# Performance work log

Measured on AMD Instinct MI355X. Metric: run time of the kernel, lower is better.

The kernel has to match this reference:

```python
import jax, jax.numpy as jnp
import numpy as np

B = 500_000
N = 6          # n_neurons
STEPS = 10     # spiking update loop length
SUBSTEPS = 8   # TwoCompColumn substeps
NOISE_STD = 0.3
I_TONIC = -1.0
# Izhikevich 'RS' parameters
IZ_A, IZ_B, IZ_C, IZ_D = 0.02, 0.2, -65.0, 8.0
V_THRESH = 30.0
RATE_ALPHA = 0.1   # rate EMA
PC_TAU = 0.5       # compartment relaxation rate


def setup_inputs() -> dict:
    key = jax.random.key(0)
    k = jax.random.split(key, 8)
    heading = jax.random.normal(k[0], (B,), dtype=jnp.float32)
    speed = jax.random.uniform(k[1], (B,), dtype=jnp.float32)
    turn_rate = jax.random.normal(k[2], (B,), dtype=jnp.float32)
    predicted_turn = jax.random.normal(k[3], (B,), dtype=jnp.float32)
    predicted_speed = jax.random.uniform(k[4], (B,), dtype=jnp.float32)
    noise = jax.random.normal(k[5], (STEPS, B, N), dtype=jnp.float32)
    # Izhikevich resting state around v=-65, u=b*v, with small jitter
    v0 = -65.0 + 2.0 * jax.random.normal(k[6], (B, N), dtype=jnp.float32)
    u0 = IZ_B * v0
    rate0 = jnp.zeros((B, N), dtype=jnp.float32)
    return {
        "heading": heading, "speed": speed, "turn_rate": turn_rate,
        "predicted_turn": predicted_turn, "predicted_speed": predicted_speed,
        "noise": noise, "v0": v0, "u0": u0, "rate0": rate0,
    }


def reference(heading, speed, turn_rate, predicted_turn, predicted_speed,
              noise, v0, u0, rate0):
    # heading is carried for API fidelity; original forward never uses it.
    del heading
    tilt = jnp.minimum(1.0, jnp.abs(turn_rate) * speed * 0.5)          # [B]
    zero = jnp.float32(0.0)
    I = jnp.stack([
        jnp.maximum(zero, turn_rate) * 10.0,
        jnp.maximum(zero, -turn_rate) * 10.0,
        speed * 5.0,
        jnp.maximum(zero, -speed + 0.5) * 5.0,
        tilt * 8.0,
        tilt * 8.0,
    ], axis=-1)                                                        # [B, N]

    def izh_step(carry, nz):
        v, u, r = carry                                                # each [B, N]
        i_tot = I + nz * NOISE_STD + I_TONIC
        v = v + (0.04 * v * v + 5.0 * v + 140.0 - u + i_tot)
        u = u + IZ_A * (IZ_B * v - u)
        fired = v >= V_THRESH
        spk = fired.astype(v.dtype)
        v = jnp.where(fired, IZ_C, v)
        u = u + spk * IZ_D
        r = r * (1.0 - RATE_ALPHA) + spk * RATE_ALPHA
        return (v, u, r), None

    (_, _, rate), _ = jax.lax.scan(izh_step, (v0, u0, rate0), noise)
    rate_mean = jnp.mean(rate, axis=-1)                                # [B]

    # TwoCompColumn: basal tracks sensory, apical tracks prediction
    sensory = jnp.stack([turn_rate, speed], axis=-1)                   # [B, 2]
    prediction = jnp.stack([predicted_turn, predicted_speed], axis=-1) # [B, 2]

    def pc_step(carry, _):
        vb, va = carry
        vb = vb + PC_TAU * (sensory - vb)
        va = va + PC_TAU * (prediction - va)
        return (vb, va), None

    (vb, va), _ = jax.lax.scan(pc_step,
                               (jnp.zeros_like(sensory), jnp.zeros_like(prediction)),
                               None, length=SUBSTEPS)
    pe = vb - va                                                       # [B, 2]
    precision = 1.0 / (1.0 + pe * pe)                                  # [B, 2]
    free_energy = 0.5 * jnp.sum(precision * pe * pe, axis=-1)          # [B]
    pe_w = 0.7 * pe[..., 0] + 0.3 * pe[..., 1]                         # [B]
    prec_mean = jnp.mean(precision, axis=-1)                           # [B]
    postural = -prec_mean * pe_w * 0.3                                 # [B]

    # [B, 6]: (tilt, rate, postural_correction, prediction_error, precision, free_energy)
    return jnp.stack([tilt, rate_mean, postural, pe_w, prec_mean, free_energy], axis=-1)
```

## Files before the change

### kernel.cpp

```cpp
#include <hip/hip_runtime.h>

#define STEPS 10
#define NN 6

__global__ __launch_bounds__(256) void spiking_vestibular_kernel(
    const float* __restrict__ speed,
    const float* __restrict__ turn_rate,
    const float* __restrict__ predicted_turn,
    const float* __restrict__ predicted_speed,
    const float* __restrict__ noise,
    const float* __restrict__ v0,
    const float* __restrict__ u0,
    const float* __restrict__ rate0,
    float* __restrict__ out,
    int B)
{
#pragma clang fp contract(off)
    int b = blockIdx.x * blockDim.x + threadIdx.x;
    if (b >= B) return;

    float tr = turn_rate[b];
    float sp = speed[b];
    float pt = predicted_turn[b];
    float ps = predicted_speed[b];

    float tilt = fminf(1.0f, fabsf(tr) * sp * 0.5f);

    float I[NN];
    I[0] = fmaxf(0.0f, tr) * 10.0f;
    I[1] = fmaxf(0.0f, -tr) * 10.0f;
    I[2] = sp * 5.0f;
    I[3] = fmaxf(0.0f, -sp + 0.5f) * 5.0f;
    I[4] = tilt * 8.0f;
    I[5] = tilt * 8.0f;

    size_t base6 = (size_t)b * NN;

    float v[NN], u[NN], r[NN];
    {
        const float2* p = reinterpret_cast<const float2*>(v0 + base6);
        float2 a0 = p[0], a1 = p[1], a2 = p[2];
        v[0] = a0.x; v[1] = a0.y; v[2] = a1.x; v[3] = a1.y; v[4] = a2.x; v[5] = a2.y;
    }
    {
        const float2* p = reinterpret_cast<const float2*>(u0 + base6);
        float2 a0 = p[0], a1 = p[1], a2 = p[2];
        u[0] = a0.x; u[1] = a0.y; u[2] = a1.x; u[3] = a1.y; u[4] = a2.x; u[5] = a2.y;
    }
    {
        const float2* p = reinterpret_cast<const float2*>(rate0 + base6);
        float2 a0 = p[0], a1 = p[1], a2 = p[2];
        r[0] = a0.x; r[1] = a0.y; r[2] = a1.x; r[3] = a1.y; r[4] = a2.x; r[5] = a2.y;
    }

    for (int t = 0; t < STEPS; ++t) {
        const float2* p = reinterpret_cast<const float2*>(noise + ((size_t)t * (size_t)B + (size_t)b) * NN);
        float2 n0 = p[0], n1 = p[1], n2 = p[2];
        float nz[NN] = { n0.x, n0.y, n1.x, n1.y, n2.x, n2.y };
#pragma unroll
        for (int n = 0; n < NN; ++n) {
            float i_tot = I[n] + nz[n] * 0.3f + (-1.0f);
            float vv = v[n];
            float un = u[n];
            vv = vv + (((((0.04f * vv) * vv) + (5.0f * vv)) + 140.0f) - un + i_tot);
            un = un + 0.02f * ((0.2f * vv) - un);
            bool fired = (vv >= 30.0f);
            float spk = fired ? 1.0f : 0.0f;
            vv = fired ? -65.0f : vv;
            un = un + spk * 8.0f;
            r[n] = r[n] * 0.9f + spk * 0.1f;
            v[n] = vv;
            u[n] = un;
        }
    }

    float rsum = ((((r[0] + r[1]) + r[2]) + r[3]) + r[4]) + r[5];
    float rate_mean = rsum / 6.0f;

    float vb0 = 0.0f, vb1 = 0.0f, va0 = 0.0f, va1 = 0.0f;
#pragma unroll
    for (int k = 0; k < 8; ++k) {
        vb0 = vb0 + 0.5f * (tr - vb0);
        vb1 = vb1 + 0.5f * (sp - vb1);
        va0 = va0 + 0.5f * (pt - va0);
        va1 = va1 + 0.5f * (ps - va1);
    }
    float pe0 = vb0 - va0;
    float pe1 = vb1 - va1;
    float prec0 = 1.0f / (1.0f + pe0 * pe0);
    float prec1 = 1.0f / (1.0f + pe1 * pe1);
    float fe = 0.5f * (((prec0 * pe0) * pe0) + ((prec1 * pe1) * pe1));
    float pe_w = 0.7f * pe0 + 0.3f * pe1;
    float prec_mean = (prec0 + prec1) / 2.0f;
    float postural = (-prec_mean) * pe_w * 0.3f;

    float2* o = reinterpret_cast<float2*>(out + base6);
    o[0] = make_float2(tilt, rate_mean);
    o[1] = make_float2(postural, pe_w);
    o[2] = make_float2(prec_mean, fe);
}

extern "C" void kernel_launch(void* const* d_in, const int* in_sizes, int n_in,
                              void* d_out, int out_size, void* d_ws, size_t ws_size,
                              hipStream_t stream) {
    const float* speed           = (const float*)d_in[1];
    const float* turn_rate       = (const float*)d_in[2];
    const float* predicted_turn  = (const float*)d_in[3];
    const float* predicted_speed = (const float*)d_in[4];
    const float* noise           = (const float*)d_in[5];
    const float* v0              = (const float*)d_in[6];
    const float* u0              = (const float*)d_in[7];
    const float* rate0           = (const float*)d_in[8];
    float* out                   = (float*)d_out;

    int B = in_sizes[1];
    int block = 256;
    int grid = (B + block - 1) / block;
    spiking_vestibular_kernel<<<grid, block, 0, stream>>>(
        speed, turn_rate, predicted_turn, predicted_speed,
        noise, v0, u0, rate0, out, B);
}
```

Baseline: 221.9 us.

## Split each batch element across four lanes handling neuron pairs

Each batch element is now processed by four threads. Three of them each own a pair of neurons, and the fourth duplicates the first pair's work, so the wave stays aligned. All noise loads are hoisted ahead of the loop so they can be in flight together, and the rate sum is reduced with lane shuffles. This gives more parallelism and lanes reading contiguous float2 data, which should coalesce memory traffic better in this memory-bound kernel. The cost is one quarter of the lanes doing wasted work, plus a redundant prediction-error computation in every lane.

Measured after the change: 219.2 us. Within noise of the previous version (-1.2%).

```diff
diff --git a/kernel.cpp b/kernel.cpp
--- a/kernel.cpp
+++ b/kernel.cpp
@@ -1,7 +1,6 @@
 #include <hip/hip_runtime.h>
 
 #define STEPS 10
-#define NN 6
 
 __global__ __launch_bounds__(256) void spiking_vestibular_kernel(
     const float* __restrict__ speed,
@@ -16,77 +15,85 @@
     int B)
 {
 #pragma clang fp contract(off)
-    int b = blockIdx.x * blockDim.x + threadIdx.x;
+    int tid = blockIdx.x * blockDim.x + threadIdx.x;
+    int b = tid >> 2;
+    int g = tid & 3;
     if (b >= B) return;
+
+    size_t base6 = (size_t)b * 6;
+    int goff = (g == 3) ? 0 : (2 * g);
+
+    float2 nz[STEPS];
+#pragma unroll
+    for (int t = 0; t < STEPS; ++t)
+        nz[t] = *reinterpret_cast<const float2*>(noise + (size_t)t * (size_t)B * 6 + base6 + goff);
+
+    float2 v2 = *reinterpret_cast<const float2*>(v0    + base6 + goff);
+    float2 u2 = *reinterpret_cast<const float2*>(u0    + base6 + goff);
+    float2 r2 = *reinterpret_cast<const float2*>(rate0 + base6 + goff);
 
     float tr = turn_rate[b];
     float sp = speed[b];
     float pt = predicted_turn[b];
     float ps = predicted_speed[b];
 
-    float tilt = fminf(1.0f, fabsf(tr) * sp * 0.5f);
+    float tilt = fminf(1.0f, (fabsf(tr) * sp) * 0.5f);
 
-    float I[NN];
-    I[0] = fmaxf(0.0f, tr) * 10.0f;
-    I[1] = fmaxf(0.0f, -tr) * 10.0f;
-    I[2] = sp * 5.0f;
-    I[3] = fmaxf(0.0f, -sp + 0.5f) * 5.0f;
-    I[4] = tilt * 8.0f;
-    I[5] = tilt * 8.0f;
+    float t8 = tilt * 8.0f;
+    float Ia = (g == 0) ? fmaxf(0.0f, tr) * 10.0f
+             : (g == 1) ? sp * 5.0f
+             : t8;
+    float Ib = (g == 0) ? fmaxf(0.0f, -tr) * 10.0f
+             : (g == 1) ? fmaxf(0.0f, -sp + 0.5f) * 5.0f
+             : t8;
 
-    size_t base6 = (size_t)b * NN;
+    float va = v2.x, vb = v2.y;
+    float ua = u2.x, ub = u2.y;
+    float ra = r2.x, rb = r2.y;
 
-    float v[NN], u[NN], r[NN];
-    {
-        const float2* p = reinterpret_cast<const float2*>(v0 + base6);
-        float2 a0 = p[0], a1 = p[1], a2 = p[2];
-        v[0] = a0.x; v[1] = a0.y; v[2] = a1.x; v[3] = a1.y; v[4] = a2.x; v[5] = a2.y;
-    }
-    {
-        const float2* p = reinterpret_cast<const float2*>(u0 + base6);
-        float2 a0 = p[0], a1 = p[1], a2 = p[2];
-        u[0] = a0.x; u[1] = a0.y; u[2] = a1.x; u[3] = a1.y; u[4] = a2.x; u[5] = a2.y;
-    }
-    {
-        const float2* p = reinterpret_cast<const float2*>(rate0 + base6);
-        float2 a0 = p[0], a1 = p[1], a2 = p[2];
-        r[0] = a0.x; r[1] = a0.y; r[2] = a1.x; r[3] = a1.y; r[4] = a2.x; r[5] = a2.y;
-    }
-
+#pragma unroll
     for (int t = 0; t < STEPS; ++t) {
-        const float2* p = reinterpret_cast<const float2*>(noise + ((size_t)t * (size_t)B + (size_t)b) * NN);
-        float2 n0 = p[0], n1 = p[1], n2 = p[2];
-        float nz[NN] = { n0.x, n0.y, n1.x, n1.y, n2.x, n2.y };
-#pragma unroll
-        for (int n = 0; n < NN; ++n) {
-            float i_tot = I[n] + nz[n] * 0.3f + (-1.0f);
-            float vv = v[n];
-            float un = u[n];
+        {
+            float i_tot = Ia + nz[t].x * 0.3f + (-1.0f);
+            float vv = va, un = ua;
             vv = vv + (((((0.04f * vv) * vv) + (5.0f * vv)) + 140.0f) - un + i_tot);
             un = un + 0.02f * ((0.2f * vv) - un);
             bool fired = (vv >= 30.0f);
             float spk = fired ? 1.0f : 0.0f;
             vv = fired ? -65.0f : vv;
             un = un + spk * 8.0f;
-            r[n] = r[n] * 0.9f + spk * 0.1f;
-            v[n] = vv;
-            u[n] = un;
+            ra = ra * 0.9f + spk * 0.1f;
+            va = vv; ua = un;
+        }
+        {
+            float i_tot = Ib + nz[t].y * 0.3f + (-1.0f);
+            float vv = vb, un = ub;
+            vv = vv + (((((0.04f * vv) * vv) + (5.0f * vv)) + 140.0f) - un + i_tot);
+            un = un + 0.02f * ((0.2f * vv) - un);
+            bool fired = (vv >= 30.0f);
+            float spk = fired ? 1.0f : 0.0f;
+            vv = fired ? -65.0f : vv;
+            un = un + spk * 8.0f;
+            rb = rb * 0.9f + spk * 0.1f;
+            vb = vv; ub = un;
         }
     }
 
-    float rsum = ((((r[0] + r[1]) + r[2]) + r[3]) + r[4]) + r[5];
-    float rate_mean = rsum / 6.0f;
+    float s  = ra + rb;
+    float s1 = __shfl_down(s, 1, 4);
+    float s2 = __shfl_down(s, 2, 4);
+    float rate_mean = ((s + s1) + s2) / 6.0f;
 
-    float vb0 = 0.0f, vb1 = 0.0f, va0 = 0.0f, va1 = 0.0f;
+    float cb0 = 0.0f, cb1 = 0.0f, ca0 = 0.0f, ca1 = 0.0f;
 #pragma unroll
     for (int k = 0; k < 8; ++k) {
-        vb0 = vb0 + 0.5f * (tr - vb0);
-        vb1 = vb1 + 0.5f * (sp - vb1);
-        va0 = va0 + 0.5f * (pt - va0);
-        va1 = va1 + 0.5f * (ps - va1);
+        cb0 = cb0 + 0.5f * (tr - cb0);
+        cb1 = cb1 + 0.5f * (sp - cb1);
+        ca0 = ca0 + 0.5f * (pt - ca0);
+        ca1 = ca1 + 0.5f * (ps - ca1);
     }
-    float pe0 = vb0 - va0;
-    float pe1 = vb1 - va1;
+    float pe0 = cb0 - ca0;
+    float pe1 = cb1 - ca1;
     float prec0 = 1.0f / (1.0f + pe0 * pe0);
     float prec1 = 1.0f / (1.0f + pe1 * pe1);
     float fe = 0.5f * (((prec0 * pe0) * pe0) + ((prec1 * pe1) * pe1));
@@ -94,10 +101,12 @@
     float prec_mean = (prec0 + prec1) / 2.0f;
     float postural = (-prec_mean) * pe_w * 0.3f;
 
-    float2* o = reinterpret_cast<float2*>(out + base6);
-    o[0] = make_float2(tilt, rate_mean);
-    o[1] = make_float2(postural, pe_w);
-    o[2] = make_float2(prec_mean, fe);
+    if (g < 3) {
+        float2 o = (g == 0) ? make_float2(tilt, rate_mean)
+                 : (g == 1) ? make_float2(postural, pe_w)
+                 :            make_float2(prec_mean, fe);
+        *reinterpret_cast<float2*>(out + base6 + 2 * g) = o;
+    }
 }
 
 extern "C" void kernel_launch(void* const* d_in, const int* in_sizes, int n_in,
@@ -114,8 +123,9 @@
     float* out                   = (float*)d_out;
 
     int B = in_sizes[1];
+    long long total = (long long)B * 4;
     int block = 256;
-    int grid = (B + block - 1) / block;
+    int grid = (int)((total + block - 1) / block);
     spiking_vestibular_kernel<<<grid, block, 0, stream>>>(
         speed, turn_rate, predicted_turn, predicted_speed,
         noise, v0, u0, rate0, out, B);
```

## Stage noise and state through LDS with async global_load_lds double buffering

Applied to the files above, without the earlier changes.

Replaces per-thread strided float2 loads of noise, v0, u0 and rate0 with wave-cooperative 16-byte global_load_lds copies into shared-memory slabs. Noise timesteps are double-buffered, with the load for step t+2 issued after step t finishes. The goal is fully coalesced global reads and overlap of memory traffic with compute. In exchange it adds a block-wide barrier every step, uses 60KB of LDS per 512-thread block (which limits occupancy), and clamps tail chunk addresses.

Result: slower. 227.6 us (+2.6%).

```diff
diff --git a/kernel.cpp b/kernel.cpp
--- a/kernel.cpp
+++ b/kernel.cpp
@@ -1,9 +1,18 @@
 #include <hip/hip_runtime.h>
 
 #define STEPS 10
-#define NN 6
+#define EPB 512
+#define BLOCK 512
+#define SLAB_F 3072
+#define CHUNK_F 256
+#define NCHUNK 12
 
-__global__ __launch_bounds__(256) void spiking_vestibular_kernel(
+#define GLOAD_LDS16(gp, lp)                                            \
+    __builtin_amdgcn_global_load_lds(                                  \
+        (const __attribute__((address_space(1))) void*)(gp),           \
+        (__attribute__((address_space(3))) void*)(lp), 16, 0, 0)
+
+__global__ __launch_bounds__(BLOCK) void spiking_vestibular_kernel(
     const float* __restrict__ speed,
     const float* __restrict__ turn_rate,
     const float* __restrict__ predicted_turn,
@@ -16,17 +25,60 @@
     int B)
 {
 #pragma clang fp contract(off)
-    int b = blockIdx.x * blockDim.x + threadIdx.x;
-    if (b >= B) return;
+    __shared__ float smem[5 * SLAB_F];
 
-    float tr = turn_rate[b];
-    float sp = speed[b];
-    float pt = predicted_turn[b];
-    float ps = predicted_speed[b];
+    const int tid = threadIdx.x;
+    const int wv  = tid >> 6;
+    const int ln  = tid & 63;
+    const long long b0 = (long long)blockIdx.x * EPB;
+    const long long nzLim = (long long)STEPS * B * 6 - CHUNK_F;
+    const long long stLim = (long long)B * 6 - CHUNK_F;
 
-    float tilt = fminf(1.0f, fabsf(tr) * sp * 0.5f);
+    auto stage = [&](const float* gbase, long long gstart, long long glim,
+                     float* lbase) {
+        for (int c = wv; c < NCHUNK; c += 8) {
+            long long fs = gstart + (long long)c * CHUNK_F;
+            if (fs > glim) fs = glim;
+            GLOAD_LDS16(gbase + fs + ln * 4, lbase + c * CHUNK_F);
+        }
+    };
 
-    float I[NN];
+    stage(noise, ((long long)0 * B + b0) * 6, nzLim, smem);
+    stage(noise, ((long long)1 * B + b0) * 6, nzLim, smem + SLAB_F);
+    stage(v0,    b0 * 6, stLim, smem + 2 * SLAB_F);
+    stage(u0,    b0 * 6, stLim, smem + 3 * SLAB_F);
+    stage(rate0, b0 * 6, stLim, smem + 4 * SLAB_F);
+    __syncthreads();
+
+    const long long b = b0 + tid;
+    const bool valid = (b < B);
+    const long long bc = valid ? b : (long long)(B - 1);
+
+    float v[6], u[6], r[6];
+    {
+        const float2* p = reinterpret_cast<const float2*>(&smem[2 * SLAB_F + tid * 6]);
+        float2 a0 = p[0], a1 = p[1], a2 = p[2];
+        v[0]=a0.x; v[1]=a0.y; v[2]=a1.x; v[3]=a1.y; v[4]=a2.x; v[5]=a2.y;
+    }
+    {
+        const float2* p = reinterpret_cast<const float2*>(&smem[3 * SLAB_F + tid * 6]);
+        float2 a0 = p[0], a1 = p[1], a2 = p[2];
+        u[0]=a0.x; u[1]=a0.y; u[2]=a1.x; u[3]=a1.y; u[4]=a2.x; u[5]=a2.y;
+    }
+    {
+        const float2* p = reinterpret_cast<const float2*>(&smem[4 * SLAB_F + tid * 6]);
+        float2 a0 = p[0], a1 = p[1], a2 = p[2];
+        r[0]=a0.x; r[1]=a0.y; r[2]=a1.x; r[3]=a1.y; r[4]=a2.x; r[5]=a2.y;
+    }
+
+    float tr = turn_rate[bc];
+    float sp = speed[bc];
+    float pt = predicted_turn[bc];
+    float ps = predicted_speed[bc];
+
+    float tilt = fminf(1.0f, (fabsf(tr) * sp) * 0.5f);
+
+    float I[6];
     I[0] = fmaxf(0.0f, tr) * 10.0f;
     I[1] = fmaxf(0.0f, -tr) * 10.0f;
     I[2] = sp * 5.0f;
@@ -34,31 +86,17 @@
     I[4] = tilt * 8.0f;
     I[5] = tilt * 8.0f;
 
-    size_t base6 = (size_t)b * NN;
-
-    float v[NN], u[NN], r[NN];
-    {
-        const float2* p = reinterpret_cast<const float2*>(v0 + base6);
-        float2 a0 = p[0], a1 = p[1], a2 = p[2];
-        v[0] = a0.x; v[1] = a0.y; v[2] = a1.x; v[3] = a1.y; v[4] = a2.x; v[5] = a2.y;
-    }
-    {
-        const float2* p = reinterpret_cast<const float2*>(u0 + base6);
-        float2 a0 = p[0], a1 = p[1], a2 = p[2];
-        u[0] = a0.x; u[1] = a0.y; u[2] = a1.x; u[3] = a1.y; u[4] = a2.x; u[5] = a2.y;
-    }
-    {
-        const float2* p = reinterpret_cast<const float2*>(rate0 + base6);
-        float2 a0 = p[0], a1 = p[1], a2 = p[2];
-        r[0] = a0.x; r[1] = a0.y; r[2] = a1.x; r[3] = a1.y; r[4] = a2.x; r[5] = a2.y;
-    }
-
+#pragma unroll
     for (int t = 0; t < STEPS; ++t) {
-        const float2* p = reinterpret_cast<const float2*>(noise + ((size_t)t * (size_t)B + (size_t)b) * NN);
-        float2 n0 = p[0], n1 = p[1], n2 = p[2];
-        float nz[NN] = { n0.x, n0.y, n1.x, n1.y, n2.x, n2.y };
+        const float* nb = smem + (t & 1) * SLAB_F;
+        float2 n0, n1, n2;
+        {
+            const float2* p = reinterpret_cast<const float2*>(&nb[tid * 6]);
+            n0 = p[0]; n1 = p[1]; n2 = p[2];
+        }
+        float nz[6] = { n0.x, n0.y, n1.x, n1.y, n2.x, n2.y };
 #pragma unroll
-        for (int n = 0; n < NN; ++n) {
+        for (int n = 0; n < 6; ++n) {
             float i_tot = I[n] + nz[n] * 0.3f + (-1.0f);
             float vv = v[n];
             float un = u[n];
@@ -72,21 +110,25 @@
             v[n] = vv;
             u[n] = un;
         }
+        __syncthreads();
+        if (t + 2 < STEPS)
+            stage(noise, ((long long)(t + 2) * B + b0) * 6, nzLim,
+                  smem + (t & 1) * SLAB_F);
     }
 
     float rsum = ((((r[0] + r[1]) + r[2]) + r[3]) + r[4]) + r[5];
     float rate_mean = rsum / 6.0f;
 
-    float vb0 = 0.0f, vb1 = 0.0f, va0 = 0.0f, va1 = 0.0f;
+    float cb0 = 0.0f, cb1 = 0.0f, ca0 = 0.0f, ca1 = 0.0f;
 #pragma unroll
     for (int k = 0; k < 8; ++k) {
-        vb0 = vb0 + 0.5f * (tr - vb0);
-        vb1 = vb1 + 0.5f * (sp - vb1);
-        va0 = va0 + 0.5f * (pt - va0);
-        va1 = va1 + 0.5f * (ps - va1);
+        cb0 = cb0 + 0.5f * (tr - cb0);
+        cb1 = cb1 + 0.5f * (sp - cb1);
+        ca0 = ca0 + 0.5f * (pt - ca0);
+        ca1 = ca1 + 0.5f * (ps - ca1);
     }
-    float pe0 = vb0 - va0;
-    float pe1 = vb1 - va1;
+    float pe0 = cb0 - ca0;
+    float pe1 = cb1 - ca1;
     float prec0 = 1.0f / (1.0f + pe0 * pe0);
     float prec1 = 1.0f / (1.0f + pe1 * pe1);
     float fe = 0.5f * (((prec0 * pe0) * pe0) + ((prec1 * pe1) * pe1));
@@ -94,10 +136,12 @@
     float prec_mean = (prec0 + prec1) / 2.0f;
     float postural = (-prec_mean) * pe_w * 0.3f;
 
-    float2* o = reinterpret_cast<float2*>(out + base6);
-    o[0] = make_float2(tilt, rate_mean);
-    o[1] = make_float2(postural, pe_w);
-    o[2] = make_float2(prec_mean, fe);
+    if (valid) {
+        float2* o = reinterpret_cast<float2*>(out + (size_t)b * 6);
+        o[0] = make_float2(tilt, rate_mean);
+        o[1] = make_float2(postural, pe_w);
+        o[2] = make_float2(prec_mean, fe);
+    }
 }
 
 extern "C" void kernel_launch(void* const* d_in, const int* in_sizes, int n_in,
@@ -114,9 +158,8 @@
     float* out                   = (float*)d_out;
 
     int B = in_sizes[1];
-    int block = 256;
-    int grid = (B + block - 1) / block;
-    spiking_vestibular_kernel<<<grid, block, 0, stream>>>(
+    int grid = (B + EPB - 1) / EPB;
+    spiking_vestibular_kernel<<<grid, BLOCK, 0, stream>>>(
         speed, turn_rate, predicted_turn, predicted_speed,
         noise, v0, u0, rate0, out, B);
 }
```

## Remap threads so three lanes share a batch pair with 16-byte vector accesses

Applied to the files above, without the earlier changes.

Each group of three lanes handles two batch elements (12 floats), and each lane loads and stores aligned float4 chunks with nontemporal hints instead of float2 pieces. All ten noise steps are prefetched up front behind a sched barrier, and the row rate sum is finished with a lane shuffle. The aim is wider, fully coalesced memory transactions and more loads in flight for this bandwidth-bound kernel. The cost is one idle lane per wave, duplicated scalar work across the three lanes, and the assumption that B is even, since an odd final element would be dropped.

Result: faster. 211.5 us (-4.7%).

```diff
diff --git a/kernel.cpp b/kernel.cpp
--- a/kernel.cpp
+++ b/kernel.cpp
@@ -1,9 +1,11 @@
 #include <hip/hip_runtime.h>
 
 #define STEPS 10
-#define NN 6
 
-__global__ __launch_bounds__(256) void spiking_vestibular_kernel(
+typedef float vf2 __attribute__((ext_vector_type(2)));
+typedef float vf4 __attribute__((ext_vector_type(4)));
+
+__global__ __launch_bounds__(256, 4) void spiking_vestibular_kernel(
     const float* __restrict__ speed,
     const float* __restrict__ turn_rate,
     const float* __restrict__ predicted_turn,
@@ -16,88 +18,132 @@
     int B)
 {
 #pragma clang fp contract(off)
-    int b = blockIdx.x * blockDim.x + threadIdx.x;
-    if (b >= B) return;
+    const int wv = threadIdx.x >> 6;
+    const int l  = threadIdx.x & 63;
+    int q = l / 3;
+    int k = l - 3 * q;
+    const bool passenger = (l == 63);
+    if (passenger) { q = 20; k = 0; }
 
-    float tr = turn_rate[b];
-    float sp = speed[b];
-    float pt = predicted_turn[b];
-    float ps = predicted_speed[b];
+    const long long P = (long long)(B >> 1);
+    long long p = (long long)blockIdx.x * 84 + wv * 21 + q;
+    const bool valid = (p < P) && !passenger;
+    if (p >= P) p = P - 1;
 
-    float tilt = fminf(1.0f, fabsf(tr) * sp * 0.5f);
+    const long long row = p * 12;
+    const int ko = k * 4;
 
-    float I[NN];
-    I[0] = fmaxf(0.0f, tr) * 10.0f;
-    I[1] = fmaxf(0.0f, -tr) * 10.0f;
-    I[2] = sp * 5.0f;
-    I[3] = fmaxf(0.0f, -sp + 0.5f) * 5.0f;
-    I[4] = tilt * 8.0f;
-    I[5] = tilt * 8.0f;
+    vf4 nz[STEPS];
+#pragma unroll
+    for (int t = 0; t < STEPS; ++t)
+        nz[t] = __builtin_nontemporal_load(
+            reinterpret_cast<const vf4*>(noise + (long long)t * B * 6 + row + ko));
+    vf4 vz = __builtin_nontemporal_load(reinterpret_cast<const vf4*>(v0    + row + ko));
+    vf4 uz = __builtin_nontemporal_load(reinterpret_cast<const vf4*>(u0    + row + ko));
+    vf4 rz = __builtin_nontemporal_load(reinterpret_cast<const vf4*>(rate0 + row + ko));
+    vf2 tr2 = *reinterpret_cast<const vf2*>(turn_rate       + 2 * p);
+    vf2 sp2 = *reinterpret_cast<const vf2*>(speed           + 2 * p);
+    vf2 pt2 = *reinterpret_cast<const vf2*>(predicted_turn  + 2 * p);
+    vf2 ps2 = *reinterpret_cast<const vf2*>(predicted_speed + 2 * p);
 
-    size_t base6 = (size_t)b * NN;
+    __builtin_amdgcn_sched_barrier(0);
 
-    float v[NN], u[NN], r[NN];
-    {
-        const float2* p = reinterpret_cast<const float2*>(v0 + base6);
-        float2 a0 = p[0], a1 = p[1], a2 = p[2];
-        v[0] = a0.x; v[1] = a0.y; v[2] = a1.x; v[3] = a1.y; v[4] = a2.x; v[5] = a2.y;
-    }
-    {
-        const float2* p = reinterpret_cast<const float2*>(u0 + base6);
-        float2 a0 = p[0], a1 = p[1], a2 = p[2];
-        u[0] = a0.x; u[1] = a0.y; u[2] = a1.x; u[3] = a1.y; u[4] = a2.x; u[5] = a2.y;
-    }
-    {
-        const float2* p = reinterpret_cast<const float2*>(rate0 + base6);
-        float2 a0 = p[0], a1 = p[1], a2 = p[2];
-        r[0] = a0.x; r[1] = a0.y; r[2] = a1.x; r[3] = a1.y; r[4] = a2.x; r[5] = a2.y;
+    const float trA = tr2.x, trB = tr2.y;
+    const float spA = sp2.x, spB = sp2.y;
+    const float ptA = pt2.x, ptB = pt2.y;
+    const float psA = ps2.x, psB = ps2.y;
+
+    const float tiltA = fminf(1.0f, (fabsf(trA) * spA) * 0.5f);
+    const float tiltB = fminf(1.0f, (fabsf(trB) * spB) * 0.5f);
+
+    float I0, I1, I2, I3;
+    if (k == 0) {
+        I0 = fmaxf(0.0f, trA) * 10.0f;
+        I1 = fmaxf(0.0f, -trA) * 10.0f;
+        I2 = spA * 5.0f;
+        I3 = fmaxf(0.0f, -spA + 0.5f) * 5.0f;
+    } else if (k == 1) {
+        I0 = tiltA * 8.0f;
+        I1 = tiltA * 8.0f;
+        I2 = fmaxf(0.0f, trB) * 10.0f;
+        I3 = fmaxf(0.0f, -trB) * 10.0f;
+    } else {
+        I0 = spB * 5.0f;
+        I1 = fmaxf(0.0f, -spB + 0.5f) * 5.0f;
+        I2 = tiltB * 8.0f;
+        I3 = tiltB * 8.0f;
     }
 
-    for (int t = 0; t < STEPS; ++t) {
-        const float2* p = reinterpret_cast<const float2*>(noise + ((size_t)t * (size_t)B + (size_t)b) * NN);
-        float2 n0 = p[0], n1 = p[1], n2 = p[2];
-        float nz[NN] = { n0.x, n0.y, n1.x, n1.y, n2.x, n2.y };
-#pragma unroll
-        for (int n = 0; n < NN; ++n) {
-            float i_tot = I[n] + nz[n] * 0.3f + (-1.0f);
-            float vv = v[n];
-            float un = u[n];
-            vv = vv + (((((0.04f * vv) * vv) + (5.0f * vv)) + 140.0f) - un + i_tot);
-            un = un + 0.02f * ((0.2f * vv) - un);
-            bool fired = (vv >= 30.0f);
-            float spk = fired ? 1.0f : 0.0f;
-            vv = fired ? -65.0f : vv;
-            un = un + spk * 8.0f;
-            r[n] = r[n] * 0.9f + spk * 0.1f;
-            v[n] = vv;
-            u[n] = un;
-        }
+    float v0r = vz.x, v1r = vz.y, v2r = vz.z, v3r = vz.w;
+    float u0r = uz.x, u1r = uz.y, u2r = uz.z, u3r = uz.w;
+    float r0r = rz.x, r1r = rz.y, r2r = rz.z, r3r = rz.w;
+
+#define IZH(Ix, vv_, uu_, rr_, nzc)                                            \
+    {                                                                          \
+        float i_tot = Ix + (nzc) * 0.3f + (-1.0f);                             \
+        float vv = vv_, un = uu_;                                              \
+        vv = vv + (((((0.04f * vv) * vv) + (5.0f * vv)) + 140.0f) - un + i_tot);\
+        un = un + 0.02f * ((0.2f * vv) - un);                                  \
+        bool fired = (vv >= 30.0f);                                            \
+        float spk = fired ? 1.0f : 0.0f;                                       \
+        vv = fired ? -65.0f : vv;                                              \
+        un = un + spk * 8.0f;                                                  \
+        rr_ = rr_ * 0.9f + spk * 0.1f;                                         \
+        vv_ = vv; uu_ = un;                                                    \
     }
 
-    float rsum = ((((r[0] + r[1]) + r[2]) + r[3]) + r[4]) + r[5];
-    float rate_mean = rsum / 6.0f;
+#pragma unroll
+    for (int t = 0; t < STEPS; ++t) {
+        IZH(I0, v0r, u0r, r0r, nz[t].x);
+        IZH(I1, v1r, u1r, r1r, nz[t].y);
+        IZH(I2, v2r, u2r, r2r, nz[t].z);
+        IZH(I3, v3r, u3r, r3r, nz[t].w);
+    }
+#undef IZH
 
-    float vb0 = 0.0f, vb1 = 0.0f, va0 = 0.0f, va1 = 0.0f;
+    float s4 = ((r0r + r1r) + r2r) + r3r;
+    float pA = (k == 0) ? s4 : (k == 1) ? (r0r + r1r) : 0.0f;
+    float pB = (k == 2) ? s4 : (k == 1) ? (r2r + r3r) : 0.0f;
+    float pA_n = __shfl(pA, l + 1, 64);
+    float pB_n = __shfl(pB, l + 1, 64);
+    float rateA = (pA + pA_n) / 6.0f;
+    float rateB = (pB + pB_n) / 6.0f;
+
+    float Ab0 = 0.0f, Ab1 = 0.0f, Aa0 = 0.0f, Aa1 = 0.0f;
+    float Bb0 = 0.0f, Bb1 = 0.0f, Ba0 = 0.0f, Ba1 = 0.0f;
 #pragma unroll
-    for (int k = 0; k < 8; ++k) {
-        vb0 = vb0 + 0.5f * (tr - vb0);
-        vb1 = vb1 + 0.5f * (sp - vb1);
-        va0 = va0 + 0.5f * (pt - va0);
-        va1 = va1 + 0.5f * (ps - va1);
+    for (int it = 0; it < 8; ++it) {
+        Ab0 = Ab0 + 0.5f * (trA - Ab0);
+        Ab1 = Ab1 + 0.5f * (spA - Ab1);
+        Aa0 = Aa0 + 0.5f * (ptA - Aa0);
+        Aa1 = Aa1 + 0.5f * (psA - Aa1);
+        Bb0 = Bb0 + 0.5f * (trB - Bb0);
+        Bb1 = Bb1 + 0.5f * (spB - Bb1);
+        Ba0 = Ba0 + 0.5f * (ptB - Ba0);
+        Ba1 = Ba1 + 0.5f * (psB - Ba1);
     }
-    float pe0 = vb0 - va0;
-    float pe1 = vb1 - va1;
-    float prec0 = 1.0f / (1.0f + pe0 * pe0);
-    float prec1 = 1.0f / (1.0f + pe1 * pe1);
-    float fe = 0.5f * (((prec0 * pe0) * pe0) + ((prec1 * pe1) * pe1));
-    float pe_w = 0.7f * pe0 + 0.3f * pe1;
-    float prec_mean = (prec0 + prec1) / 2.0f;
-    float postural = (-prec_mean) * pe_w * 0.3f;
+    float peA0 = Ab0 - Aa0, peA1 = Ab1 - Aa1;
+    float peB0 = Bb0 - Ba0, peB1 = Bb1 - Ba1;
+    float prA0 = 1.0f / (1.0f + peA0 * peA0);
+    float prA1 = 1.0f / (1.0f + peA1 * peA1);
+    float prB0 = 1.0f / (1.0f + peB0 * peB0);
+    float prB1 = 1.0f / (1.0f + peB1 * peB1);
+    float feA = 0.5f * (((prA0 * peA0) * peA0) + ((prA1 * peA1) * peA1));
+    float feB = 0.5f * (((prB0 * peB0) * peB0) + ((prB1 * peB1) * peB1));
+    float pewA = 0.7f * peA0 + 0.3f * peA1;
+    float pewB = 0.7f * peB0 + 0.3f * peB1;
+    float pmA = (prA0 + prA1) / 2.0f;
+    float pmB = (prB0 + prB1) / 2.0f;
+    float postA = (-pmA) * pewA * 0.3f;
+    float postB = (-pmB) * pewB * 0.3f;
 
-    float2* o = reinterpret_cast<float2*>(out + base6);
-    o[0] = make_float2(tilt, rate_mean);
-    o[1] = make_float2(postural, pe_w);
-    o[2] = make_float2(prec_mean, fe);
+    vf4 o;
+    if (k == 0)      { o.x = tiltA; o.y = rateA; o.z = postA; o.w = pewA; }
+    else if (k == 1) { o.x = pmA;   o.y = feA;   o.z = tiltB; o.w = rateB; }
+    else             { o.x = postB; o.y = pewB;  o.z = pmB;   o.w = feB; }
+
+    if (valid)
+        __builtin_nontemporal_store(o, reinterpret_cast<vf4*>(out + row + ko));
 }
 
 extern "C" void kernel_launch(void* const* d_in, const int* in_sizes, int n_in,
@@ -114,9 +160,10 @@
     float* out                   = (float*)d_out;
 
     int B = in_sizes[1];
-    int block = 256;
-    int grid = (B + block - 1) / block;
-    spiking_vestibular_kernel<<<grid, block, 0, stream>>>(
+    long long pairs = (long long)(B >> 1);
+    long long ppb = 84;
+    int grid = (int)((pairs + ppb - 1) / ppb);
+    spiking_vestibular_kernel<<<grid, 256, 0, stream>>>(
         speed, turn_rate, predicted_turn, predicted_speed,
         noise, v0, u0, rate0, out, B);
 }
```
